# Kernel optimization log

Hardware: AMD Instinct MI355X
Metric: run time of the kernel (lower is better)

## Reference

```python
import jax, jax.numpy as jnp
import numpy as np

T_, B_, DIM, NB, D, H_, W_ = 4, 4, 256, 16, 16, 32, 32
VTH_L1_LOW = VTH_L1_HIGH = 0.5
EPS = 1e-5

# ---- surrogate-gradient spike (ATan surrogate, alpha=2.0, spikingjelly default) ----
@jax.custom_vjp
def spike(x):
    return (x >= 0).astype(x.dtype)

def _spk_fwd(x):
    return spike(x), x

def _spk_bwd(x, g):
    a = 2.0
    return (g * (a / 2.0) / (1.0 + (jnp.pi / 2.0 * a * x) ** 2),)

spike.defvjp(_spk_fwd, _spk_bwd)

def lif(x, tau=2.0, vth=1.0):
    # MultiStepLIFNode: v += (x - v)/tau; fire at vth; hard reset (detach_reset)
    def step(v, xt):
        v = v + (xt - v) / tau
        s = spike(v - vth)
        v = v * (1.0 - jax.lax.stop_gradient(s))
        return v, s
    _, s = jax.lax.scan(step, jnp.zeros_like(x[0]), x)
    return s

def haar_mat(n):
    m = np.zeros((n, n), np.float32)
    s = 1.0 / np.sqrt(2.0)
    for i in range(n // 2):
        m[i, 2 * i] = s; m[i, 2 * i + 1] = s          # low-pass rows
        m[n // 2 + i, 2 * i] = s; m[n // 2 + i, 2 * i + 1] = -s  # high-pass rows
    return jnp.asarray(m)

def bn(x, g, b):  # training-mode BatchNorm2d over (N,C,H,W)
    mu = jnp.mean(x, axis=(0, 2, 3), keepdims=True)
    var = jnp.var(x, axis=(0, 2, 3), keepdims=True)
    return g.reshape(1, -1, 1, 1) * (x - mu) * jax.lax.rsqrt(var + EPS) + b.reshape(1, -1, 1, 1)

def conv(x, w, b):
    y = jax.lax.conv_general_dilated(x, w, (1, 1), 'SAME',
                                     dimension_numbers=('NCHW', 'OIHW', 'NCHW'))
    return y + b.reshape(1, -1, 1, 1)

def band_gate(c, vth, tau):
    # coefficient spiking threshold then channel-energy sparsity gate
    c = c * spike(jnp.abs(c) - vth)
    E = jnp.mean(c * c, axis=(-2, -1), keepdims=True)  # per (T,B,C) energy
    return c * (E > tau).astype(c.dtype)

def _forward(x, haar_weight, conv1_w, conv1_b, conv2_w, conv2_b,
             bn_fwd_g, bn_fwd_b, bn_mul_g, bn_mul_b, bn_inv_g, bn_inv_b,
             bn_c1_g, bn_c1_b, bn_c2_g, bn_c2_b):
    T, B, C, H, W = x.shape
    HmW, HmH = haar_mat(W), haar_mat(H)
    Hh, Wh, TB = H // 2, W // 2, T * B
    s = lif(x)
    # ---- level-1 Haar along W ----
    y = jnp.einsum('vw,tbchw->tbchv', HmW, s)
    low, high = y[..., :Wh], y[..., Wh:]
    low = low * spike(jnp.abs(low) - VTH_L1_LOW)
    high = high * spike(jnp.abs(high) - VTH_L1_HIGH)
    l1 = jnp.concatenate([low, high], axis=2)  # (T,B,2C,H,Wh)
    l1 = bn(l1.reshape(TB, 2 * C, H, Wh), bn_fwd_g, bn_fwd_b).reshape(T, B, 2 * C, H, Wh)
    # ---- level-2 Haar along H + per-band sparsity ----
    lo, hi = l1[:, :, :C], l1[:, :, C:]
    zlo = jnp.einsum('vh,tbchw->tbcvw', HmH, lo)
    zhi = jnp.einsum('vh,tbchw->tbcvw', HmH, hi)
    LL = band_gate(zlo[..., :Hh, :], 0.5, 0.01)
    HL = band_gate(zlo[..., Hh:, :], 0.5, 0.02)
    LH = band_gate(zhi[..., :Hh, :], 0.5, 0.02)
    HH = band_gate(zhi[..., Hh:, :], 0.5, 0.05)
    l2 = jnp.concatenate([LL, HL, LH, HH], axis=2)  # (T,B,4C,Hh,Wh)
    l2 = bn(l2.reshape(TB, 4 * C, Hh, Wh), bn_mul_g, bn_mul_b)
    # ---- block-diagonal multiply ----
    h = l2.reshape(TB, NB, 4 * D, Hh, Wh).transpose(0, 3, 4, 1, 2)  # (TB,Hh,Wh,NB,4D)
    parts = [jnp.einsum('thwbd,bdk->thwbk', h[..., i * D:(i + 1) * D], haar_weight)
             for i in range(4)]
    h = jnp.concatenate(parts, axis=-1)
    h = h.reshape(TB, Hh, Wh, 4 * C).transpose(0, 3, 1, 2).reshape(T, B, 4 * C, Hh, Wh)
    # ---- inverse Haar ----
    LLc, HLc, LHc, HHc = h[:, :, :C], h[:, :, C:2 * C], h[:, :, 2 * C:3 * C], h[:, :, 3 * C:]
    lo = jnp.einsum('vh,tbcvw->tbchw', HmH, jnp.concatenate([LLc, HLc], axis=-2))
    hi = jnp.einsum('vh,tbcvw->tbchw', HmH, jnp.concatenate([LHc, HHc], axis=-2))
    rec = jnp.einsum('vw,tbchv->tbchw', HmW, jnp.concatenate([lo, hi], axis=-1))
    rec = bn(rec.reshape(TB, C, H, W), bn_inv_g, bn_inv_b).reshape(T, B, C, H, W)
    # ---- conv residual paths over block channels ----
    xr = s.reshape(TB * NB, D, H, W)
    c1 = bn(conv(xr, conv1_w, conv1_b).reshape(TB, C, H, W), bn_c1_g, bn_c1_b).reshape(T, B, C, H, W)
    c2 = bn(conv(xr, conv2_w, conv2_b).reshape(TB, C, H, W), bn_c2_g, bn_c2_b).reshape(T, B, C, H, W)
    return rec + c1 + c2

def setup_inputs() -> dict:
    key = jax.random.key(0)
    ks = jax.random.split(key, 4)
    return {
        'x': jax.random.normal(ks[0], (T_, B_, DIM, H_, W_), jnp.float32),
        'haar_weight': 0.02 * jax.random.normal(ks[1], (NB, D, D), jnp.float32),
        'conv1_w': 0.1 * jax.random.normal(ks[2], (D, D, 1, 1), jnp.float32),
        'conv1_b': jnp.zeros((D,), jnp.float32),
        'conv2_w': 0.05 * jax.random.normal(ks[3], (D, D, 3, 3), jnp.float32),
        'conv2_b': jnp.zeros((D,), jnp.float32),
        'bn_fwd_g': jnp.ones((2 * DIM,), jnp.float32), 'bn_fwd_b': jnp.zeros((2 * DIM,), jnp.float32),
        'bn_mul_g': jnp.ones((4 * DIM,), jnp.float32), 'bn_mul_b': jnp.zeros((4 * DIM,), jnp.float32),
        'bn_inv_g': jnp.ones((DIM,), jnp.float32), 'bn_inv_b': jnp.zeros((DIM,), jnp.float32),
        'bn_c1_g': jnp.ones((DIM,), jnp.float32), 'bn_c1_b': jnp.zeros((DIM,), jnp.float32),
        'bn_c2_g': jnp.ones((DIM,), jnp.float32), 'bn_c2_b': jnp.zeros((DIM,), jnp.float32),
    }

def reference(x, haar_weight, conv1_w, conv1_b, conv2_w, conv2_b,
              bn_fwd_g, bn_fwd_b, bn_mul_g, bn_mul_b, bn_inv_g, bn_inv_b,
              bn_c1_g, bn_c1_b, bn_c2_g, bn_c2_b):
    return _forward(x, haar_weight, conv1_w, conv1_b, conv2_w, conv2_b,
                    bn_fwd_g, bn_fwd_b, bn_mul_g, bn_mul_b, bn_inv_g, bn_inv_b,
                    bn_c1_g, bn_c1_b, bn_c2_g, bn_c2_b)
```

## Files before the change

kernel.cpp:

```cpp
#include <hip/hip_runtime.h>
#include <hip/hip_bf16.h>

#define T_ 4
#define B_ 4
#define C_ 256
#define H_ 32
#define W_ 32
#define TB_ 16
#define Hh_ 16
#define Wh_ 16
#define INVS2 0.70710678118654752440f
#define EPSBN 1e-5f

#define OFF_HW   0
#define OFF_W1   4096
#define OFF_B1   4352
#define OFF_W2   4368
#define OFF_B2   6672
#define OFF_G1   6688
#define OFF_BE1  7200
#define OFF_G2   7712
#define OFF_BE2  8736
#define OFF_G3   9760
#define OFF_BE3  10016
#define OFF_G4   10272
#define OFF_BE4  10528
#define OFF_G5   10784
#define OFF_BE5  11040
#define W_TOTAL  11296
#define NSUMS    4608

struct WPtrs { const void* p[15]; };

typedef __attribute__((ext_vector_type(8))) short short8;
typedef __attribute__((ext_vector_type(4))) float f32x4;

__device__ inline float bf2f(__hip_bfloat16 v) { return __bfloat162float(v); }
__device__ inline float bfu(unsigned short u) { return __uint_as_float((unsigned)u << 16); }

__global__ __launch_bounds__(256) void k_prep(const unsigned short* __restrict__ xr,
                                              WPtrs wp,
                                              __hip_bfloat16* __restrict__ wc,
                                              float* __restrict__ sums,
                                              int* __restrict__ flag) {
    int tid = threadIdx.x;
    int cnt = 0;
    for (int i = tid; i < 2048; i += 256) {
        int e = (xr[i] >> 7) & 0xFF;
        if (e >= 134) cnt++;
    }
    for (int o = 1; o < 64; o <<= 1) cnt += __shfl_xor(cnt, o, 64);
    __shared__ int sh[4];
    if ((tid & 63) == 0) sh[tid >> 6] = cnt;
    __syncthreads();
    int f = (sh[0] + sh[1] + sh[2] + sh[3] >= 32) ? 1 : 0;
    if (blockIdx.x == 0 && tid == 0) *flag = f;

    const int sizes[15] = {4096, 256, 16, 2304, 16, 512, 512, 1024, 1024,
                           256, 256, 256, 256, 256, 256};
    int i = blockIdx.x * 256 + tid;
    if (i < W_TOTAL) {
        int seg = 0, off = 0;
        while (i >= off + sizes[seg]) { off += sizes[seg]; seg++; }
        int j = i - off;
        float v = f ? ((const float*)wp.p[seg])[j]
                    : bf2f(((const __hip_bfloat16*)wp.p[seg])[j]);
        wc[i] = __float2bfloat16(v);
    }
    if (i < NSUMS) sums[i] = 0.f;
}

__global__ __launch_bounds__(256) void k_lifhaar(const void* __restrict__ x_,
                                                 const int* __restrict__ flag,
                                                 unsigned char* __restrict__ s,
                                                 float* __restrict__ sums1) {
    int bid = blockIdx.x;
    int tid = threadIdx.x;
    int half = bid & 1;
    int c = (bid >> 1) & 255;
    int b = bid >> 9;
    int wp = tid & 15;
    int hl = tid >> 4;
    int h = half * 16 + hl;
    int f = *flag;
    const float* xf = (const float*)x_;
    const unsigned int* xb = (const unsigned int*)x_;
    int n = ((b * 256 + c) * 32 + h) * 32 + 2 * wp;

    float v0 = 0.f, v1 = 0.f;
    float aL = 0.f, qL = 0.f, aH = 0.f, qH = 0.f;
    #pragma unroll
    for (int t = 0; t < T_; ++t) {
        size_t idx = (size_t)t * 1048576 + n;
        float x0, x1;
        if (f) {
            float2 xx = *(const float2*)(xf + idx);
            x0 = xx.x; x1 = xx.y;
        } else {
            unsigned int u = xb[idx >> 1];
            x0 = __uint_as_float(u << 16);
            x1 = __uint_as_float(u & 0xffff0000u);
        }
        v0 += (x0 - v0) * 0.5f;
        v1 += (x1 - v1) * 0.5f;
        float s0 = (v0 >= 1.f) ? 1.f : 0.f;
        float s1 = (v1 >= 1.f) ? 1.f : 0.f;
        v0 *= (1.f - s0);
        v1 *= (1.f - s1);
        int tb = t * 4 + b;
        ((uchar2*)s)[(size_t)(tb * 256 + c) * 512 + h * 16 + wp] =
            make_uchar2((unsigned char)s0, (unsigned char)s1);
        float cl = s0 + s1, ch = s0 - s1;
        aL += cl; qL += cl * cl; aH += ch; qH += ch * ch;
    }
    for (int o = 1; o < 64; o <<= 1) {
        aL += __shfl_xor(aL, o, 64); qL += __shfl_xor(qL, o, 64);
        aH += __shfl_xor(aH, o, 64); qH += __shfl_xor(qH, o, 64);
    }
    __shared__ float part[4][4];
    int lane = tid & 63, wv = tid >> 6;
    if (lane == 0) {
        part[wv][0] = aL; part[wv][1] = qL; part[wv][2] = aH; part[wv][3] = qH;
    }
    __syncthreads();
    if (tid < 4) {
        float tot = part[0][tid] + part[1][tid] + part[2][tid] + part[3][tid];
        const int offs[4] = {0, 512, 256, 768};
        atomicAdd(&sums1[offs[tid] + c], tot);
    }
}

__global__ __launch_bounds__(256) void k_stage2(const unsigned char* __restrict__ s,
                                                const float* __restrict__ sums1,
                                                const __hip_bfloat16* __restrict__ wc,
                                                float* __restrict__ stats,
                                                __hip_bfloat16* __restrict__ l2) {
    int blk = blockIdx.x;
    int c = blk & 255;
    int tb = blk >> 8;
    int tid = threadIdx.x;
    int lane = tid & 63, wv = tid >> 6;

    const float nrm = 1.f / 8192.f;
    float mL = sums1[c] * INVS2 * nrm;
    float vL = fmaxf(sums1[512 + c] * 0.5f * nrm - mL * mL, 0.f);
    float sL = bf2f(wc[OFF_G1 + c]) * rsqrtf(vL + EPSBN);
    float tL = bf2f(wc[OFF_BE1 + c]) - mL * sL;
    float mH = sums1[256 + c] * INVS2 * nrm;
    float vH = fmaxf(sums1[768 + c] * 0.5f * nrm - mH * mH, 0.f);
    float sH = bf2f(wc[OFF_G1 + 256 + c]) * rsqrtf(vH + EPSBN);
    float tH = bf2f(wc[OFF_BE1 + 256 + c]) - mH * sH;
    float slo = sL * INVS2, shi = sH * INVS2;

    int w = tid & 15, v = tid >> 4;
    const uchar2* sp = (const uchar2*)(s + ((size_t)(tb * 256 + c)) * 1024);
    uchar2 pa = sp[(2 * v) * 16 + w];
    uchar2 pb = sp[(2 * v + 1) * 16 + w];
    float lt = (float)(pa.x + pa.y) * slo + tL;
    float lb = (float)(pb.x + pb.y) * slo + tL;
    float ht = (float)((int)pa.x - (int)pa.y) * shi + tH;
    float hb = (float)((int)pb.x - (int)pb.y) * shi + tH;

    float zLL = (lt + lb) * INVS2;
    float zHL = (lt - lb) * INVS2;
    float zLH = (ht + hb) * INVS2;
    float zHH = (ht - hb) * INVS2;
    zLL = (fabsf(zLL) - 0.5f >= 0.f) ? zLL : 0.f;
    zHL = (fabsf(zHL) - 0.5f >= 0.f) ? zHL : 0.f;
    zLH = (fabsf(zLH) - 0.5f >= 0.f) ? zLH : 0.f;
    zHH = (fabsf(zHH) - 0.5f >= 0.f) ? zHH : 0.f;

    float r0 = zLL, r1 = zHL, r2 = zLH, r3 = zHH;
    float q0 = zLL * zLL, q1 = zHL * zHL, q2 = zLH * zLH, q3 = zHH * zHH;
    for (int o = 1; o < 64; o <<= 1) {
        r0 += __shfl_xor(r0, o, 64); r1 += __shfl_xor(r1, o, 64);
        r2 += __shfl_xor(r2, o, 64); r3 += __shfl_xor(r3, o, 64);
        q0 += __shfl_xor(q0, o, 64); q1 += __shfl_xor(q1, o, 64);
        q2 += __shfl_xor(q2, o, 64); q3 += __shfl_xor(q3, o, 64);
    }
    __shared__ float part[4][8];
    if (lane == 0) {
        part[wv][0] = r0; part[wv][1] = r1; part[wv][2] = r2; part[wv][3] = r3;
        part[wv][4] = q0; part[wv][5] = q1; part[wv][6] = q2; part[wv][7] = q3;
    }
    __syncthreads();
    float S0 = part[0][0] + part[1][0] + part[2][0] + part[3][0];
    float S1 = part[0][1] + part[1][1] + part[2][1] + part[3][1];
    float S2 = part[0][2] + part[1][2] + part[2][2] + part[3][2];
    float S3 = part[0][3] + part[1][3] + part[2][3] + part[3][3];
    float Q0 = part[0][4] + part[1][4] + part[2][4] + part[3][4];
    float Q1 = part[0][5] + part[1][5] + part[2][5] + part[3][5];
    float Q2 = part[0][6] + part[1][6] + part[2][6] + part[3][6];
    float Q3 = part[0][7] + part[1][7] + part[2][7] + part[3][7];
    float fLL = (Q0 * (1.f / 256.f) > 0.01f) ? 1.f : 0.f;
    float fHL = (Q1 * (1.f / 256.f) > 0.02f) ? 1.f : 0.f;
    float fLH = (Q2 * (1.f / 256.f) > 0.02f) ? 1.f : 0.f;
    float fHH = (Q3 * (1.f / 256.f) > 0.05f) ? 1.f : 0.f;

    float* sums2 = stats + 1024;
    if (tid < 8) {
        const int cho[8] = {0, 1024, 256, 1280, 512, 1536, 768, 1792};
        const float vals[8] = {fLL * S0, fLL * Q0, fHL * S1, fHL * Q1,
                               fLH * S2, fLH * Q2, fHH * S3, fHH * Q3};
        atomicAdd(&sums2[cho[tid] + c], vals[tid]);
    }

    size_t ob = (((size_t)tb * 1024) + c) * 256 + tid;
    l2[ob]               = __float2bfloat16(zLL * fLL);
    l2[ob + 256u * 256u] = __float2bfloat16(zHL * fHL);
    l2[ob + 512u * 256u] = __float2bfloat16(zLH * fLH);
    l2[ob + 768u * 256u] = __float2bfloat16(zHH * fHH);
}

struct SharedU {
    union {
        struct {
            short lo[1025 * 8];
            short hi[1025 * 8];
            unsigned short w2s[2304];
            unsigned short w1s[256];
            unsigned short bs[32];
            float parts[4][4][16];
        } cv;
        struct {
            float wt[4][16][16];
            float bsc[64], bsh[64];
            float parts2[4][32];
        } mi;
    };
};

__global__ __launch_bounds__(256) void k_convmix(const unsigned char* __restrict__ s,
                                                 const __hip_bfloat16* __restrict__ l2,
                                                 const __hip_bfloat16* __restrict__ wc,
                                                 float* __restrict__ stats,
                                                 __hip_bfloat16* __restrict__ rec,
                                                 __hip_bfloat16* __restrict__ c1,
                                                 __hip_bfloat16* __restrict__ c2) {
    __shared__ SharedU sm;
    int bid = blockIdx.x;
    int tid = threadIdx.x;
    int lane = tid & 63, wv = tid >> 6;

    if (bid < 256) {
        int img = bid;
        const unsigned short* wr = (const unsigned short*)wc;
        for (int i = tid; i < 2304; i += 256) sm.cv.w2s[i] = wr[OFF_W2 + i];
        sm.cv.w1s[tid] = wr[OFF_W1 + tid];
        if (tid < 16) { sm.cv.bs[tid] = wr[OFF_B1 + tid]; sm.cv.bs[16 + tid] = wr[OFF_B2 + tid]; }
        if (tid < 8) {
            ((unsigned int*)sm.cv.lo)[4096 + (tid & 3)] = 0;
            ((unsigned int*)sm.cv.hi)[4096 + (tid & 3)] = 0;
        }
        {
            const unsigned int* sp = (const unsigned int*)(s + (size_t)img * 16384);
            int d2 = tid >> 5;
            int pg = tid & 31;
            unsigned int* dst = (unsigned int*)((d2 < 4) ? sm.cv.lo : sm.cv.hi);
            int dl = d2 & 3;
            #pragma unroll
            for (int p = 0; p < 8; ++p) {
                int base = p * 32 + pg;
                unsigned int u0 = sp[d2 * 512 + base];
                unsigned int u1 = sp[d2 * 512 + 256 + base];
                #pragma unroll
                for (int jj = 0; jj < 4; ++jj) {
                    int j = (jj + pg) & 3;
                    unsigned int b0 = (u0 >> (8 * j)) & 255u;
                    unsigned int b1 = (u1 >> (8 * j)) & 255u;
                    unsigned int val = (b0 ? 0x3F80u : 0u) | ((b1 ? 0x3F80u : 0u) << 16);
                    int pix = p * 128 + pg * 4 + j;
                    dst[pix * 4 + dl] = val;
                }
            }
        }
        __syncthreads();

        int m = lane & 15;
        int g = lane >> 4;
        const int tapA[5] = {0, 2, 4, 6, 8};
        const int tapB[5] = {1, 3, 5, 7, 8};

        short8 afr[5], a1f;
        #pragma unroll
        for (int p = 0; p < 5; ++p) {
            int tap = (g < 2) ? tapA[p] : tapB[p];
            short8 av;
            #pragma unroll
            for (int j = 0; j < 8; ++j) {
                int d = (g & 1) * 8 + j;
                unsigned short w = sm.cv.w2s[m * 144 + d * 9 + tap];
                if (p == 4 && g >= 2) w = 0;
                av[j] = (short)w;
            }
            afr[p] = av;
        }
        #pragma unroll
        for (int j = 0; j < 8; ++j) {
            int d = (g & 1) * 8 + j;
            a1f[j] = (g < 2) ? (short)sm.cv.w1s[m * 16 + d] : (short)0;
        }
        float bias1[4], bias2[4];
        #pragma unroll
        for (int r = 0; r < 4; ++r) {
            bias1[r] = bfu(sm.cv.bs[g * 4 + r]);
            bias2[r] = bfu(sm.cv.bs[16 + g * 4 + r]);
        }

        __hip_bfloat16* o1 = c1 + (size_t)img * 16384;
        __hip_bfloat16* o2 = c2 + (size_t)img * 16384;
        const short* bsrc = (g & 1) ? sm.cv.hi : sm.cv.lo;

        float cs1[4] = {0, 0, 0, 0}, cq1[4] = {0, 0, 0, 0};
        float cs2[4] = {0, 0, 0, 0}, cq2[4] = {0, 0, 0, 0};

        for (int t = wv * 16; t < wv * 16 + 16; ++t) {
            int h = t >> 1;
            int w0 = (t & 1) << 4;
            f32x4 acc2 = {0.f, 0.f, 0.f, 0.f};
            f32x4 acc1 = {0.f, 0.f, 0.f, 0.f};
            #pragma unroll
            for (int p = 0; p < 5; ++p) {
                int tap = (g < 2) ? tapA[p] : tapB[p];
                int row = h + tap / 3 - 1;
                int col = w0 + m + (tap % 3) - 1;
                bool ok = ((unsigned)row < 32u) && ((unsigned)col < 32u);
                int idx = ok ? (row * 32 + col) : 1024;
                short8 bv = *(const short8*)&bsrc[idx * 8];
                acc2 = __builtin_amdgcn_mfma_f32_16x16x32_bf16(afr[p], bv, acc2, 0, 0, 0);
                if (p == 2)
                    acc1 = __builtin_amdgcn_mfma_f32_16x16x32_bf16(a1f, bv, acc1, 0, 0, 0);
            }
            int pix = h * 32 + w0 + m;
            #pragma unroll
            for (int r = 0; r < 4; ++r) {
                int k = g * 4 + r;
                float y1 = acc1[r] + bias1[r];
                float y2 = acc2[r] + bias2[r];
                o1[(size_t)k * 1024 + pix] = __float2bfloat16(y1);
                o2[(size_t)k * 1024 + pix] = __float2bfloat16(y2);
                cs1[r] += y1; cq1[r] += y1 * y1;
                cs2[r] += y2; cq2[r] += y2 * y2;
            }
        }
        #pragma unroll
        for (int o = 1; o < 16; o <<= 1) {
            #pragma unroll
            for (int r = 0; r < 4; ++r) {
                cs1[r] += __shfl_xor(cs1[r], o, 64);
                cq1[r] += __shfl_xor(cq1[r], o, 64);
                cs2[r] += __shfl_xor(cs2[r], o, 64);
                cq2[r] += __shfl_xor(cq2[r], o, 64);
            }
        }
        if (m == 0) {
            #pragma unroll
            for (int r = 0; r < 4; ++r) {
                sm.cv.parts[wv][g][r * 4 + 0] = cs1[r];
                sm.cv.parts[wv][g][r * 4 + 1] = cq1[r];
                sm.cv.parts[wv][g][r * 4 + 2] = cs2[r];
                sm.cv.parts[wv][g][r * 4 + 3] = cq2[r];
            }
        }
        __syncthreads();
        if (tid < 64) {
            int gg = tid >> 4, r = (tid >> 2) & 3, which = tid & 3;
            float tot = sm.cv.parts[0][gg][r * 4 + which] + sm.cv.parts[1][gg][r * 4 + which]
                      + sm.cv.parts[2][gg][r * 4 + which] + sm.cv.parts[3][gg][r * 4 + which];
            int ch = (img & 15) * 16 + gg * 4 + r;
            const int base[4] = {3584, 3840, 4096, 4352};
            atomicAdd(&stats[base[which] + ch], tot);
        }
    } else {
        int mb = bid - 256;
        int cg = mb & 15;
        int tb = mb >> 4;
        const float* sums2 = stats + 1024;

        for (int i = tid; i < 1024; i += 256) {
            int q = i >> 8, rem = i & 255, d = rem >> 4, k = rem & 15;
            int nb = q * 4 + (cg >> 2);
            sm.mi.wt[q][d][k] = bf2f(wc[OFF_HW + nb * 256 + d * 16 + k]);
        }
        if (tid < 64) {
            int q = tid >> 4, d = tid & 15;
            int ch = q * 256 + cg * 16 + d;
            float m = sums2[ch] * (1.f / 4096.f);
            float var = fmaxf(sums2[1024 + ch] * (1.f / 4096.f) - m * m, 0.f);
            float sc = bf2f(wc[OFF_G2 + ch]) * rsqrtf(var + EPSBN);
            sm.mi.bsc[tid] = sc;
            sm.mi.bsh[tid] = bf2f(wc[OFF_BE2 + ch]) - m * sc;
        }
        __syncthreads();

        float h[4][16];
        #pragma unroll
        for (int q = 0; q < 4; ++q)
            #pragma unroll
            for (int k = 0; k < 16; ++k) h[q][k] = 0.f;

        int p = tid;
        #pragma unroll
        for (int q = 0; q < 4; ++q) {
            const __hip_bfloat16* base =
                l2 + ((size_t)tb * 1024 + q * 256 + cg * 16) * 256 + p;
            #pragma unroll
            for (int d = 0; d < 16; ++d) {
                float xv = bf2f(base[d * 256]) * sm.mi.bsc[q * 16 + d] + sm.mi.bsh[q * 16 + d];
                #pragma unroll
                for (int k = 0; k < 16; ++k)
                    h[q][k] = fmaf(xv, sm.mi.wt[q][d][k], h[q][k]);
            }
        }

        int uh = tid >> 4, uw = tid & 15;
        __hip_bfloat16* ob = rec + ((size_t)tb * 256 + cg * 16) * 1024;
        float sk[16], qk[16];
        #pragma unroll
        for (int k = 0; k < 16; ++k) {
            float LL = h[0][k], HL = h[1][k], LH = h[2][k], HH = h[3][k];
            float v00 = 0.5f * (LL + HL + LH + HH);
            float v01 = 0.5f * (LL + HL - LH - HH);
            float v10 = 0.5f * (LL - HL + LH - HH);
            float v11 = 0.5f * (LL - HL - LH + HH);
            __hip_bfloat162 top, bot;
            top.x = __float2bfloat16(v00); top.y = __float2bfloat16(v01);
            bot.x = __float2bfloat16(v10); bot.y = __float2bfloat16(v11);
            *(__hip_bfloat162*)(ob + (size_t)k * 1024 + (2 * uh) * 32 + 2 * uw) = top;
            *(__hip_bfloat162*)(ob + (size_t)k * 1024 + (2 * uh + 1) * 32 + 2 * uw) = bot;
            sk[k] = v00 + v01 + v10 + v11;
            qk[k] = v00 * v00 + v01 * v01 + v10 * v10 + v11 * v11;
        }
        for (int o = 1; o < 64; o <<= 1) {
            #pragma unroll
            for (int k = 0; k < 16; ++k) {
                sk[k] += __shfl_xor(sk[k], o, 64);
                qk[k] += __shfl_xor(qk[k], o, 64);
            }
        }
        if (lane == 0) {
            #pragma unroll
            for (int k = 0; k < 16; ++k) {
                sm.mi.parts2[wv][k * 2]     = sk[k];
                sm.mi.parts2[wv][k * 2 + 1] = qk[k];
            }
        }
        __syncthreads();
        if (tid < 32) {
            int k = tid >> 1, which = tid & 1;
            float tot = sm.mi.parts2[0][tid] + sm.mi.parts2[1][tid]
                      + sm.mi.parts2[2][tid] + sm.mi.parts2[3][tid];
            atomicAdd(&stats[3072 + which * 256 + cg * 16 + k], tot);
        }
    }
}

__global__ __launch_bounds__(256) void k_final(const __hip_bfloat16* __restrict__ rec,
                                               const __hip_bfloat16* __restrict__ c1,
                                               const __hip_bfloat16* __restrict__ c2,
                                               const float* __restrict__ stats,
                                               const __hip_bfloat16* __restrict__ wc,
                                               const int* __restrict__ flag,
                                               void* __restrict__ out_) {
    int n8 = blockIdx.x * 256 + threadIdx.x;
    int c = ((n8 * 8) >> 10) & 255;
    const float inv = 1.f / 16384.f;
    float m3 = stats[3072 + c] * inv;
    float v3 = fmaxf(stats[3328 + c] * inv - m3 * m3, 0.f);
    float sc3 = bf2f(wc[OFF_G3 + c]) * rsqrtf(v3 + EPSBN);
    float sh3 = bf2f(wc[OFF_BE3 + c]) - m3 * sc3;
    float m4 = stats[3584 + c] * inv;
    float v4 = fmaxf(stats[3840 + c] * inv - m4 * m4, 0.f);
    float sc4 = bf2f(wc[OFF_G4 + c]) * rsqrtf(v4 + EPSBN);
    float sh4 = bf2f(wc[OFF_BE4 + c]) - m4 * sc4;
    float m5 = stats[4096 + c] * inv;
    float v5 = fmaxf(stats[4352 + c] * inv - m5 * m5, 0.f);
    float sc5 = bf2f(wc[OFF_G5 + c]) * rsqrtf(v5 + EPSBN);
    float sh5 = bf2f(wc[OFF_BE5 + c]) - m5 * sc5;

    short8 r = ((const short8*)rec)[n8];
    short8 a = ((const short8*)c1)[n8];
    short8 b = ((const short8*)c2)[n8];
    float v[8];
    #pragma unroll
    for (int j = 0; j < 8; ++j) {
        v[j] = bfu((unsigned short)r[j]) * sc3 + sh3
             + bfu((unsigned short)a[j]) * sc4 + sh4
             + bfu((unsigned short)b[j]) * sc5 + sh5;
    }
    if (*flag) {
        float4* o = (float4*)out_;
        o[n8 * 2]     = make_float4(v[0], v[1], v[2], v[3]);
        o[n8 * 2 + 1] = make_float4(v[4], v[5], v[6], v[7]);
    } else {
        short8 o;
        #pragma unroll
        for (int j = 0; j < 8; ++j)
            o[j] = (short)__bfloat16_as_ushort(__float2bfloat16(v[j]));
        ((short8*)out_)[n8] = o;
    }
}

extern "C" void kernel_launch(void* const* d_in, const int* in_sizes, int n_in,
                              void* d_out, int out_size, void* d_ws, size_t ws_size,
                              hipStream_t stream) {
    char* ws = (char*)d_ws;
    unsigned char* s_u8  = (unsigned char*)ws;
    __hip_bfloat16* l2   = (__hip_bfloat16*)(ws + ((size_t)8 << 20));
    __hip_bfloat16* rec  = (__hip_bfloat16*)(ws + ((size_t)16 << 20));
    __hip_bfloat16* c1   = (__hip_bfloat16*)(ws + ((size_t)24 << 20));
    __hip_bfloat16* c2   = (__hip_bfloat16*)(ws + ((size_t)32 << 20));
    __hip_bfloat16* wc   = (__hip_bfloat16*)(ws + ((size_t)40 << 20));
    float* stats         = (float*)(ws + ((size_t)40 << 20) + (64 << 10));
    int* flag            = (int*)(ws + ((size_t)40 << 20) + (128 << 10));

    WPtrs wp;
    for (int i = 0; i < 15; ++i) wp.p[i] = d_in[i + 1];

    dim3 blk(256);
    k_prep<<<dim3(45), blk, 0, stream>>>((const unsigned short*)d_in[0], wp, wc, stats, flag);
    k_lifhaar<<<dim3(2048), blk, 0, stream>>>(d_in[0], flag, s_u8, stats);
    k_stage2<<<dim3(4096), blk, 0, stream>>>(s_u8, stats, wc, stats, l2);
    k_convmix<<<dim3(512), blk, 0, stream>>>(s_u8, l2, wc, stats, rec, c1, c2);
    k_final<<<dim3(2048), blk, 0, stream>>>(rec, c1, c2, stats, wc, flag, d_out);
}
```

Before: 150.8 us.

## Remove prep kernel and replace atomic stat accumulation with per-block partial buffers

Drops the separate weight-conversion and zeroing kernel: each kernel now reads weights directly from the inputs, converting per load, and every block of k_lifhaar sniffs the input dtype itself. BatchNorm statistics are no longer accumulated with global atomicAdd into zeroed buffers. Each block writes its partial sums to a dedicated slot, and the consuming kernel reduces those partials. This removes one launch and atomic contention, at the cost of redundant dtype sniffing in every block and extra partial reductions in the consumers.

```diff
diff --git a/kernel.cpp b/kernel.cpp
--- a/kernel.cpp
+++ b/kernel.cpp
@@ -12,77 +12,45 @@
 #define INVS2 0.70710678118654752440f
 #define EPSBN 1e-5f
 
-#define OFF_HW   0
-#define OFF_W1   4096
-#define OFF_B1   4352
-#define OFF_W2   4368
-#define OFF_B2   6672
-#define OFF_G1   6688
-#define OFF_BE1  7200
-#define OFF_G2   7712
-#define OFF_BE2  8736
-#define OFF_G3   9760
-#define OFF_BE3  10016
-#define OFF_G4   10272
-#define OFF_BE4  10528
-#define OFF_G5   10784
-#define OFF_BE5  11040
-#define W_TOTAL  11296
-#define NSUMS    4608
-
-struct WPtrs { const void* p[15]; };
-
 typedef __attribute__((ext_vector_type(8))) short short8;
 typedef __attribute__((ext_vector_type(4))) float f32x4;
 
 __device__ inline float bf2f(__hip_bfloat16 v) { return __bfloat162float(v); }
 __device__ inline float bfu(unsigned short u) { return __uint_as_float((unsigned)u << 16); }
-
-__global__ __launch_bounds__(256) void k_prep(const unsigned short* __restrict__ xr,
-                                              WPtrs wp,
-                                              __hip_bfloat16* __restrict__ wc,
-                                              float* __restrict__ sums,
-                                              int* __restrict__ flag) {
+__device__ inline float wload(const void* p, int i, int f) {
+    return f ? ((const float*)p)[i] : bf2f(((const __hip_bfloat16*)p)[i]);
+}
+__device__ inline unsigned short wbits(const void* p, int i, int f) {
+    return f ? __bfloat16_as_ushort(__float2bfloat16(((const float*)p)[i]))
+             : ((const unsigned short*)p)[i];
+}
+
+__global__ __launch_bounds__(256) void k_lifhaar(const void* __restrict__ x_,
+                                                 unsigned char* __restrict__ s,
+                                                 float* __restrict__ part1,
+                                                 int* __restrict__ flag) {
+    int bid = blockIdx.x;
     int tid = threadIdx.x;
+    int lane = tid & 63, wv = tid >> 6;
+
+    const unsigned short* xr = (const unsigned short*)x_;
     int cnt = 0;
     for (int i = tid; i < 2048; i += 256) {
         int e = (xr[i] >> 7) & 0xFF;
         if (e >= 134) cnt++;
     }
     for (int o = 1; o < 64; o <<= 1) cnt += __shfl_xor(cnt, o, 64);
-    __shared__ int sh[4];
-    if ((tid & 63) == 0) sh[tid >> 6] = cnt;
+    __shared__ int snif[4];
+    if (lane == 0) snif[wv] = cnt;
     __syncthreads();
-    int f = (sh[0] + sh[1] + sh[2] + sh[3] >= 32) ? 1 : 0;
-    if (blockIdx.x == 0 && tid == 0) *flag = f;
-
-    const int sizes[15] = {4096, 256, 16, 2304, 16, 512, 512, 1024, 1024,
-                           256, 256, 256, 256, 256, 256};
-    int i = blockIdx.x * 256 + tid;
-    if (i < W_TOTAL) {
-        int seg = 0, off = 0;
-        while (i >= off + sizes[seg]) { off += sizes[seg]; seg++; }
-        int j = i - off;
-        float v = f ? ((const float*)wp.p[seg])[j]
-                    : bf2f(((const __hip_bfloat16*)wp.p[seg])[j]);
-        wc[i] = __float2bfloat16(v);
-    }
-    if (i < NSUMS) sums[i] = 0.f;
-}
-
-__global__ __launch_bounds__(256) void k_lifhaar(const void* __restrict__ x_,
-                                                 const int* __restrict__ flag,
-                                                 unsigned char* __restrict__ s,
-                                                 float* __restrict__ sums1) {
-    int bid = blockIdx.x;
-    int tid = threadIdx.x;
+    int f = (snif[0] + snif[1] + snif[2] + snif[3] >= 32) ? 1 : 0;
+    if (bid == 0 && tid == 0) *flag = f;
+
     int half = bid & 1;
     int c = (bid >> 1) & 255;
     int b = bid >> 9;
     int wp = tid & 15;
-    int hl = tid >> 4;
-    int h = half * 16 + hl;
-    int f = *flag;
+    int h = half * 16 + (tid >> 4);
     const float* xf = (const float*)x_;
     const unsigned int* xb = (const unsigned int*)x_;
     int n = ((b * 256 + c) * 32 + h) * 32 + 2 * wp;
@@ -118,38 +86,51 @@
         aH += __shfl_xor(aH, o, 64); qH += __shfl_xor(qH, o, 64);
     }
     __shared__ float part[4][4];
-    int lane = tid & 63, wv = tid >> 6;
     if (lane == 0) {
         part[wv][0] = aL; part[wv][1] = qL; part[wv][2] = aH; part[wv][3] = qH;
     }
     __syncthreads();
     if (tid < 4) {
         float tot = part[0][tid] + part[1][tid] + part[2][tid] + part[3][tid];
-        const int offs[4] = {0, 512, 256, 768};
-        atomicAdd(&sums1[offs[tid] + c], tot);
+        part1[c * 32 + (b * 2 + half) * 4 + tid] = tot;
     }
 }
 
 __global__ __launch_bounds__(256) void k_stage2(const unsigned char* __restrict__ s,
-                                                const float* __restrict__ sums1,
-                                                const __hip_bfloat16* __restrict__ wc,
-                                                float* __restrict__ stats,
+                                                const float* __restrict__ part1,
+                                                const void* __restrict__ g1p,
+                                                const void* __restrict__ be1p,
+                                                const int* __restrict__ flag,
+                                                float* __restrict__ part2,
                                                 __hip_bfloat16* __restrict__ l2) {
     int blk = blockIdx.x;
     int c = blk & 255;
     int tb = blk >> 8;
     int tid = threadIdx.x;
     int lane = tid & 63, wv = tid >> 6;
+    int f = *flag;
+
+    __shared__ float ps[32];
+    __shared__ float tot4[4];
+    if (tid < 32) ps[tid] = part1[c * 32 + tid];
+    __syncthreads();
+    if (tid < 4) {
+        float t = 0.f;
+        #pragma unroll
+        for (int k8 = 0; k8 < 8; ++k8) t += ps[k8 * 4 + tid];
+        tot4[tid] = t;
+    }
+    __syncthreads();
 
     const float nrm = 1.f / 8192.f;
-    float mL = sums1[c] * INVS2 * nrm;
-    float vL = fmaxf(sums1[512 + c] * 0.5f * nrm - mL * mL, 0.f);
-    float sL = bf2f(wc[OFF_G1 + c]) * rsqrtf(vL + EPSBN);
-    float tL = bf2f(wc[OFF_BE1 + c]) - mL * sL;
-    float mH = sums1[256 + c] * INVS2 * nrm;
-    float vH = fmaxf(sums1[768 + c] * 0.5f * nrm - mH * mH, 0.f);
-    float sH = bf2f(wc[OFF_G1 + 256 + c]) * rsqrtf(vH + EPSBN);
-    float tH = bf2f(wc[OFF_BE1 + 256 + c]) - mH * sH;
+    float mL = tot4[0] * INVS2 * nrm;
+    float vL = fmaxf(tot4[1] * 0.5f * nrm - mL * mL, 0.f);
+    float sL = wload(g1p, c, f) * rsqrtf(vL + EPSBN);
+    float tL = wload(be1p, c, f) - mL * sL;
+    float mH = tot4[2] * INVS2 * nrm;
+    float vH = fmaxf(tot4[3] * 0.5f * nrm - mH * mH, 0.f);
+    float sH = wload(g1p, 256 + c, f) * rsqrtf(vH + EPSBN);
+    float tH = wload(be1p, 256 + c, f) - mH * sH;
     float slo = sL * INVS2, shi = sH * INVS2;
 
     int w = tid & 15, v = tid >> 4;
@@ -197,12 +178,10 @@
     float fLH = (Q2 * (1.f / 256.f) > 0.02f) ? 1.f : 0.f;
     float fHH = (Q3 * (1.f / 256.f) > 0.05f) ? 1.f : 0.f;
 
-    float* sums2 = stats + 1024;
     if (tid < 8) {
-        const int cho[8] = {0, 1024, 256, 1280, 512, 1536, 768, 1792};
         const float vals[8] = {fLL * S0, fLL * Q0, fHL * S1, fHL * Q1,
                                fLH * S2, fLH * Q2, fHH * S3, fHH * Q3};
-        atomicAdd(&sums2[cho[tid] + c], vals[tid]);
+        part2[c * 128 + tb * 8 + tid] = vals[tid];
     }
 
     size_t ob = (((size_t)tb * 1024) + c) * 256 + tid;
@@ -225,6 +204,7 @@
         struct {
             float wt[4][16][16];
             float bsc[64], bsh[64];
+            float red2[128];
             float parts2[4][32];
         } mi;
     };
@@ -232,8 +212,17 @@
 
 __global__ __launch_bounds__(256) void k_convmix(const unsigned char* __restrict__ s,
                                                  const __hip_bfloat16* __restrict__ l2,
-                                                 const __hip_bfloat16* __restrict__ wc,
-                                                 float* __restrict__ stats,
+                                                 const void* __restrict__ hwp,
+                                                 const void* __restrict__ w1p,
+                                                 const void* __restrict__ b1p,
+                                                 const void* __restrict__ w2p,
+                                                 const void* __restrict__ b2p,
+                                                 const void* __restrict__ g2p,
+                                                 const void* __restrict__ be2p,
+                                                 const int* __restrict__ flag,
+                                                 const float* __restrict__ part2,
+                                                 float* __restrict__ part3,
+                                                 float* __restrict__ part45,
                                                  __hip_bfloat16* __restrict__ rec,
                                                  __hip_bfloat16* __restrict__ c1,
                                                  __hip_bfloat16* __restrict__ c2) {
@@ -241,13 +230,13 @@
     int bid = blockIdx.x;
     int tid = threadIdx.x;
     int lane = tid & 63, wv = tid >> 6;
+    int f = *flag;
 
     if (bid < 256) {
         int img = bid;
-        const unsigned short* wr = (const unsigned short*)wc;
-        for (int i = tid; i < 2304; i += 256) sm.cv.w2s[i] = wr[OFF_W2 + i];
-        sm.cv.w1s[tid] = wr[OFF_W1 + tid];
-        if (tid < 16) { sm.cv.bs[tid] = wr[OFF_B1 + tid]; sm.cv.bs[16 + tid] = wr[OFF_B2 + tid]; }
+        for (int i = tid; i < 2304; i += 256) sm.cv.w2s[i] = wbits(w2p, i, f);
+        sm.cv.w1s[tid] = wbits(w1p, tid, f);
+        if (tid < 16) { sm.cv.bs[tid] = wbits(b1p, tid, f); sm.cv.bs[16 + tid] = wbits(b2p, tid, f); }
         if (tid < 8) {
             ((unsigned int*)sm.cv.lo)[4096 + (tid & 3)] = 0;
             ((unsigned int*)sm.cv.hi)[4096 + (tid & 3)] = 0;
@@ -368,28 +357,38 @@
             float tot = sm.cv.parts[0][gg][r * 4 + which] + sm.cv.parts[1][gg][r * 4 + which]
                       + sm.cv.parts[2][gg][r * 4 + which] + sm.cv.parts[3][gg][r * 4 + which];
             int ch = (img & 15) * 16 + gg * 4 + r;
-            const int base[4] = {3584, 3840, 4096, 4352};
-            atomicAdd(&stats[base[which] + ch], tot);
+            part45[ch * 64 + (img >> 4) * 4 + which] = tot;
         }
     } else {
         int mb = bid - 256;
         int cg = mb & 15;
         int tb = mb >> 4;
-        const float* sums2 = stats + 1024;
 
         for (int i = tid; i < 1024; i += 256) {
             int q = i >> 8, rem = i & 255, d = rem >> 4, k = rem & 15;
             int nb = q * 4 + (cg >> 2);
-            sm.mi.wt[q][d][k] = bf2f(wc[OFF_HW + nb * 256 + d * 16 + k]);
-        }
+            sm.mi.wt[q][d][k] = wload(hwp, nb * 256 + d * 16 + k, f);
+        }
+        if (tid < 128) {
+            int q = tid >> 5, rest = tid & 31, d = rest >> 1, w = rest & 1;
+            int cl = cg * 16 + d;
+            float acc = 0.f;
+            #pragma unroll
+            for (int t2 = 0; t2 < 16; ++t2)
+                acc += part2[cl * 128 + t2 * 8 + q * 2 + w];
+            sm.mi.red2[q * 32 + d * 2 + w] = acc;
+        }
+        __syncthreads();
         if (tid < 64) {
             int q = tid >> 4, d = tid & 15;
             int ch = q * 256 + cg * 16 + d;
-            float m = sums2[ch] * (1.f / 4096.f);
-            float var = fmaxf(sums2[1024 + ch] * (1.f / 4096.f) - m * m, 0.f);
-            float sc = bf2f(wc[OFF_G2 + ch]) * rsqrtf(var + EPSBN);
+            float S = sm.mi.red2[q * 32 + d * 2];
+            float Q = sm.mi.red2[q * 32 + d * 2 + 1];
+            float m = S * (1.f / 4096.f);
+            float var = fmaxf(Q * (1.f / 4096.f) - m * m, 0.f);
+            float sc = wload(g2p, ch, f) * rsqrtf(var + EPSBN);
             sm.mi.bsc[tid] = sc;
-            sm.mi.bsh[tid] = bf2f(wc[OFF_BE2 + ch]) - m * sc;
+            sm.mi.bsh[tid] = wload(be2p, ch, f) - m * sc;
         }
         __syncthreads();
 
@@ -447,10 +446,10 @@
         }
         __syncthreads();
         if (tid < 32) {
-            int k = tid >> 1, which = tid & 1;
+            int k = tid >> 1, w = tid & 1;
             float tot = sm.mi.parts2[0][tid] + sm.mi.parts2[1][tid]
                       + sm.mi.parts2[2][tid] + sm.mi.parts2[3][tid];
-            atomicAdd(&stats[3072 + which * 256 + cg * 16 + k], tot);
+            part3[(cg * 16 + k) * 32 + tb * 2 + w] = tot;
         }
     }
 }
@@ -458,25 +457,48 @@
 __global__ __launch_bounds__(256) void k_final(const __hip_bfloat16* __restrict__ rec,
                                                const __hip_bfloat16* __restrict__ c1,
                                                const __hip_bfloat16* __restrict__ c2,
-                                               const float* __restrict__ stats,
-                                               const __hip_bfloat16* __restrict__ wc,
+                                               const float* __restrict__ part3,
+                                               const float* __restrict__ part45,
+                                               const void* __restrict__ g3p, const void* __restrict__ be3p,
+                                               const void* __restrict__ g4p, const void* __restrict__ be4p,
+                                               const void* __restrict__ g5p, const void* __restrict__ be5p,
                                                const int* __restrict__ flag,
                                                void* __restrict__ out_) {
-    int n8 = blockIdx.x * 256 + threadIdx.x;
-    int c = ((n8 * 8) >> 10) & 255;
-    const float inv = 1.f / 16384.f;
-    float m3 = stats[3072 + c] * inv;
-    float v3 = fmaxf(stats[3328 + c] * inv - m3 * m3, 0.f);
-    float sc3 = bf2f(wc[OFF_G3 + c]) * rsqrtf(v3 + EPSBN);
-    float sh3 = bf2f(wc[OFF_BE3 + c]) - m3 * sc3;
-    float m4 = stats[3584 + c] * inv;
-    float v4 = fmaxf(stats[3840 + c] * inv - m4 * m4, 0.f);
-    float sc4 = bf2f(wc[OFF_G4 + c]) * rsqrtf(v4 + EPSBN);
-    float sh4 = bf2f(wc[OFF_BE4 + c]) - m4 * sc4;
-    float m5 = stats[4096 + c] * inv;
-    float v5 = fmaxf(stats[4352 + c] * inv - m5 * m5, 0.f);
-    float sc5 = bf2f(wc[OFF_G5 + c]) * rsqrtf(v5 + EPSBN);
-    float sh5 = bf2f(wc[OFF_BE5 + c]) - m5 * sc5;
+    int bid = blockIdx.x;
+    int tid = threadIdx.x;
+    int f = *flag;
+
+    __shared__ float coef[2][6];
+    if (tid < 2) {
+        int c = (bid * 2 + tid) & 255;
+        float S3 = 0.f, Q3 = 0.f, S4 = 0.f, Q4 = 0.f, S5 = 0.f, Q5 = 0.f;
+        #pragma unroll
+        for (int t2 = 0; t2 < 16; ++t2) {
+            S3 += part3[c * 32 + t2 * 2];
+            Q3 += part3[c * 32 + t2 * 2 + 1];
+            S4 += part45[c * 64 + t2 * 4];
+            Q4 += part45[c * 64 + t2 * 4 + 1];
+            S5 += part45[c * 64 + t2 * 4 + 2];
+            Q5 += part45[c * 64 + t2 * 4 + 3];
+        }
+        const float inv = 1.f / 16384.f;
+        float m3 = S3 * inv, v3 = fmaxf(Q3 * inv - m3 * m3, 0.f);
+        float sc3 = wload(g3p, c, f) * rsqrtf(v3 + EPSBN);
+        float m4 = S4 * inv, v4 = fmaxf(Q4 * inv - m4 * m4, 0.f);
+        float sc4 = wload(g4p, c, f) * rsqrtf(v4 + EPSBN);
+        float m5 = S5 * inv, v5 = fmaxf(Q5 * inv - m5 * m5, 0.f);
+        float sc5 = wload(g5p, c, f) * rsqrtf(v5 + EPSBN);
+        coef[tid][0] = sc3; coef[tid][1] = wload(be3p, c, f) - m3 * sc3;
+        coef[tid][2] = sc4; coef[tid][3] = wload(be4p, c, f) - m4 * sc4;
+        coef[tid][4] = sc5; coef[tid][5] = wload(be5p, c, f) - m5 * sc5;
+    }
+    __syncthreads();
+
+    int n8 = bid * 256 + tid;
+    int cl = (tid >> 7) & 1;
+    float sc3 = coef[cl][0], sh3 = coef[cl][1];
+    float sc4 = coef[cl][2], sh4 = coef[cl][3];
+    float sc5 = coef[cl][4], sh5 = coef[cl][5];
 
     short8 r = ((const short8*)rec)[n8];
     short8 a = ((const short8*)c1)[n8];
@@ -488,7 +510,7 @@
              + bfu((unsigned short)a[j]) * sc4 + sh4
              + bfu((unsigned short)b[j]) * sc5 + sh5;
     }
-    if (*flag) {
+    if (f) {
         float4* o = (float4*)out_;
         o[n8 * 2]     = make_float4(v[0], v[1], v[2], v[3]);
         o[n8 * 2 + 1] = make_float4(v[4], v[5], v[6], v[7]);
@@ -510,17 +532,20 @@
     __hip_bfloat16* rec  = (__hip_bfloat16*)(ws + ((size_t)16 << 20));
     __hip_bfloat16* c1   = (__hip_bfloat16*)(ws + ((size_t)24 << 20));
     __hip_bfloat16* c2   = (__hip_bfloat16*)(ws + ((size_t)32 << 20));
-    __hip_bfloat16* wc   = (__hip_bfloat16*)(ws + ((size_t)40 << 20));
-    float* stats         = (float*)(ws + ((size_t)40 << 20) + (64 << 10));
-    int* flag            = (int*)(ws + ((size_t)40 << 20) + (128 << 10));
-
-    WPtrs wp;
-    for (int i = 0; i < 15; ++i) wp.p[i] = d_in[i + 1];
+    float* part1         = (float*)(ws + ((size_t)40 << 20));
+    float* part2         = (float*)(ws + ((size_t)40 << 20) + (64 << 10));
+    float* part3         = (float*)(ws + ((size_t)40 << 20) + (256 << 10));
+    float* part45        = (float*)(ws + ((size_t)40 << 20) + (320 << 10));
+    int* flag            = (int*)(ws + ((size_t)40 << 20) + (448 << 10));
 
     dim3 blk(256);
-    k_prep<<<dim3(45), blk, 0, stream>>>((const unsigned short*)d_in[0], wp, wc, stats, flag);
-    k_lifhaar<<<dim3(2048), blk, 0, stream>>>(d_in[0], flag, s_u8, stats);
-    k_stage2<<<dim3(4096), blk, 0, stream>>>(s_u8, stats, wc, stats, l2);
-    k_convmix<<<dim3(512), blk, 0, stream>>>(s_u8, l2, wc, stats, rec, c1, c2);
-    k_final<<<dim3(2048), blk, 0, stream>>>(rec, c1, c2, stats, wc, flag, d_out);
-}
+    k_lifhaar<<<dim3(2048), blk, 0, stream>>>(d_in[0], s_u8, part1, flag);
+    k_stage2<<<dim3(4096), blk, 0, stream>>>(s_u8, part1, d_in[6], d_in[7],
+                                             flag, part2, l2);
+    k_convmix<<<dim3(512), blk, 0, stream>>>(s_u8, l2, d_in[1], d_in[2], d_in[3],
+                                             d_in[4], d_in[5], d_in[8], d_in[9],
+                                             flag, part2, part3, part45, rec, c1, c2);
+    k_final<<<dim3(2048), blk, 0, stream>>>(rec, c1, c2, part3, part45,
+                                            d_in[10], d_in[11], d_in[12], d_in[13],
+                                            d_in[14], d_in[15], flag, d_out);
+}
```

Result: no change. 151.8 us (+0.6%).
